# Kernel optimization log

Hardware: AMD Instinct MI355X
Metric: run time of the kernel (lower is better)

The kernel has to match this reference:

```python
import jax, jax.numpy as jnp
import numpy as np

N_NODES = 50000
N_EDGES = 600000
N_REL = 8
D_IN = 128
D_OUT = 128


def setup_inputs() -> dict:
    key = jax.random.key(0)
    ks = jax.random.split(key, 12)
    s = 1.0 / np.sqrt(D_IN)
    s2 = 1.0 / np.sqrt(2 * D_IN)
    return {
        "x": jax.random.normal(ks[0], (N_NODES, D_IN), jnp.float32),
        "src": jax.random.randint(ks[1], (N_EDGES,), 0, N_NODES, jnp.int32),
        "dst": jax.random.randint(ks[2], (N_EDGES,), 0, N_NODES, jnp.int32),
        "etype": jax.random.randint(ks[3], (N_EDGES,), 0, N_REL, jnp.int32),
        "Wrel": jax.random.normal(ks[4], (N_REL, D_IN, D_OUT), jnp.float32) * s,
        "Wloop": jax.random.normal(ks[5], (D_IN, D_OUT), jnp.float32) * s,
        "brel": jax.random.normal(ks[6], (D_OUT,), jnp.float32) * s,
        "W1": jax.random.normal(ks[7], (2 * D_IN, 2 * D_IN), jnp.float32) * s2,
        "b1": jax.random.normal(ks[8], (2 * D_IN,), jnp.float32) * s2,
        "W2": jax.random.normal(ks[9], (2 * D_IN, D_OUT), jnp.float32) * s2,
        "b2": jax.random.normal(ks[10], (D_OUT,), jnp.float32) * s2,
    }


def rel_graph_conv(x, src, dst, etype, Wrel, Wloop, brel):
    # low_mem style: transform node features once per relation, then gather per edge.
    xW = jnp.einsum('ni,rio->rno', x, Wrel)          # [R, N, D_OUT]
    msg = xW[etype, src]                              # [E, D_OUT] gather by (rel, src)
    agg = jax.ops.segment_sum(msg, dst, num_segments=N_NODES)  # scatter-add to dst
    return agg + x @ Wloop + brel                     # self-loop + bias (DGL defaults)


def reference(x, src, dst, etype, Wrel, Wloop, brel, W1, b1, W2, b2):
    mid = rel_graph_conv(x, src, dst, etype, Wrel, Wloop, brel)
    h = jnp.concatenate([x, mid], axis=1)             # [N, 2*D_IN]
    h = jax.nn.relu(h @ W1 + b1)
    return h @ W2 + b2
```

## Files before the change

kernel.cpp:

```cpp
#include <hip/hip_runtime.h>

#define N_NODES 50000
#define N_EDGES 600000
#define N_REL 8
#define NT_PAD 50176
#define N_TILES 196

typedef __attribute__((ext_vector_type(8))) short bf16x8;
typedef __attribute__((ext_vector_type(4))) float f32x4;

__device__ __forceinline__ ushort f2b(float f) {
    union { float f; unsigned u; } v; v.f = f;
    unsigned r = v.u + 0x7FFFu + ((v.u >> 16) & 1u);
    return (ushort)(r >> 16);
}
__device__ __forceinline__ float b2f(ushort s) {
    union { unsigned u; float f; } v; v.u = ((unsigned)s) << 16;
    return v.f;
}
__device__ __forceinline__ float asf(unsigned u) {
    union { unsigned u; float f; } v; v.u = u;
    return v.f;
}


__global__ void conv_f32_bf16(const float* __restrict__ in, ushort* __restrict__ outb) {
    int i = (blockIdx.x * 256 + threadIdx.x) * 4;
    float4 f = *(const float4*)(in + i);
    ushort4 o; o.x = f2b(f.x); o.y = f2b(f.y); o.z = f2b(f.z); o.w = f2b(f.w);
    *(ushort4*)(outb + i) = o;
}

__global__ void transpose_wts3(const float* __restrict__ Wloop, const float* __restrict__ Wrel,
                               const float* __restrict__ W1, const float* __restrict__ W2,
                               ushort* __restrict__ wt) {
    int y = blockIdx.y;
    if (y == 0) {
        for (int idx = blockIdx.x * 256 + threadIdx.x; idx < 128 * 1152; idx += gridDim.x * 256) {
            int c = idx / 1152, kg = idx - c * 1152;
            float v = (kg < 1024) ? Wrel[(size_t)((kg >> 7) * 128 + (kg & 127)) * 128 + c]
                                  : Wloop[(size_t)(kg - 1024) * 128 + c];
            wt[idx] = f2b(v);
        }
    } else if (y == 1) {
        for (int idx = blockIdx.x * 256 + threadIdx.x; idx < 256 * 256; idx += gridDim.x * 256) {
            int c = idx >> 8, k = idx & 255;
            wt[147456 + idx] = f2b(W1[k * 256 + c]);
        }
    } else {
        for (int idx = blockIdx.x * 256 + threadIdx.x; idx < 128 * 256; idx += gridDim.x * 256) {
            int c = idx >> 8, k = idx & 255;
            wt[212992 + idx] = f2b(W2[k * 128 + c]);
        }
    }
}

template<int NPH, int KMODE, int AS, int CTOT, int OMODE>
__global__ __launch_bounds__(256, 4) void mfma_gemm(
        const ushort* __restrict__ A0, const ushort* __restrict__ A1,
        const ushort* __restrict__ Bt, const float* __restrict__ bias,
        void* __restrict__ outv) {
    __shared__ ushort bs[2][128 * 72];
    const int t = threadIdx.x;
    const int wave = t >> 6, lane = t & 63;
    const int lr = lane & 15, lg = lane >> 4;
    const int wr = (wave >> 1) * 32, wc = (wave & 1) * 64;
    const int row0 = blockIdx.x * 64;
    const int KTOT = NPH * 64;
    const ushort* Btb = Bt + (size_t)blockIdx.y * 128 * KTOT;
    const int sgk = (t & 7) * 8;
    const int sc0 = t >> 3;

#define STAGE_LOAD(p)                                                              \
    _Pragma("unroll")                                                              \
    for (int it = 0; it < 4; ++it)                                                 \
        sreg[it] = *(const bf16x8*)(Btb + (size_t)(sc0 + it * 32) * KTOT +         \
                                    (p) * 64 + sgk);

#define STAGE_WRITE(b)                                                             \
    _Pragma("unroll")                                                              \
    for (int it = 0; it < 4; ++it)                                                 \
        *(bf16x8*)(&bs[b][(sc0 + it * 32) * 72 + sgk]) = sreg[it];

#define LOAD_AF(p, dstf)                                                           \
    {                                                                              \
        const ushort* Ap; int as_;                                                 \
        if (KMODE == 0) {                                                          \
            if ((p) < 16) { Ap = A0 + (p) * 64;        as_ = 1024; }               \
            else          { Ap = A1 + ((p) - 16) * 64; as_ = 128;  }               \
        } else { Ap = A0 + (p) * 64; as_ = AS; }                                   \
        _Pragma("unroll")                                                          \
        for (int rt = 0; rt < 2; ++rt) {                                           \
            int ar = row0 + wr + rt * 16 + lr;                                     \
            if (ar >= N_NODES) ar = 0;                                             \
            _Pragma("unroll")                                                      \
            for (int kc = 0; kc < 2; ++kc)                                         \
                dstf[rt][kc] = *(const bf16x8*)(Ap + (size_t)ar * as_ + kc * 32 + lg * 8); \
        }                                                                          \
    }

    f32x4 acc[2][4];
#pragma unroll
    for (int rt = 0; rt < 2; ++rt)
#pragma unroll
        for (int nt = 0; nt < 4; ++nt) acc[rt][nt] = (f32x4){0.f, 0.f, 0.f, 0.f};

    bf16x8 af[2][2], afn[2][2], sreg[4];

    STAGE_LOAD(0);
    LOAD_AF(0, af);
    STAGE_WRITE(0);
    __syncthreads();

#pragma unroll
    for (int p = 0; p < NPH; ++p) {
        if (p + 1 < NPH) {
            STAGE_LOAD(p + 1);
            LOAD_AF(p + 1, afn);
        }
        const ushort* bcur = bs[p & 1];
#pragma unroll
        for (int kc = 0; kc < 2; ++kc) {
            bf16x8 bf[4];
#pragma unroll
            for (int nt = 0; nt < 4; ++nt)
                bf[nt] = *(const bf16x8*)(bcur + (wc + nt * 16 + lr) * 72 + kc * 32 + lg * 8);
#pragma unroll
            for (int rt = 0; rt < 2; ++rt)
#pragma unroll
                for (int nt = 0; nt < 4; ++nt)
                    acc[rt][nt] = __builtin_amdgcn_mfma_f32_16x16x32_bf16(af[rt][kc], bf[nt], acc[rt][nt], 0, 0, 0);
        }
        if (p + 1 < NPH) STAGE_WRITE((p + 1) & 1);
        __syncthreads();
        if (p + 1 < NPH) {
#pragma unroll
            for (int rt = 0; rt < 2; ++rt)
#pragma unroll
                for (int kc = 0; kc < 2; ++kc) af[rt][kc] = afn[rt][kc];
        }
    }

    const int colbase = blockIdx.y * 128;
#pragma unroll
    for (int rt = 0; rt < 2; ++rt) {
#pragma unroll
        for (int nt = 0; nt < 4; ++nt) {
            const int col = colbase + wc + nt * 16 + lr;
            const float bv = bias[col];
#pragma unroll
            for (int j = 0; j < 4; ++j) {
                const int r = row0 + wr + rt * 16 + lg * 4 + j;
                if (r >= N_NODES) continue;
                float vv = acc[rt][nt][j] + bv;
                if (OMODE == 0) {
                    ((float*)outv)[(size_t)r * CTOT + col] = vv;
                } else {
                    ((ushort*)outv)[(size_t)r * 128 + col] = f2b(vv);
                }
            }
        }
    }
#undef STAGE_LOAD
#undef STAGE_WRITE
#undef LOAD_AF
}

__global__ __launch_bounds__(256, 2) void mlp_fused(
        const ushort* __restrict__ xbf, const ushort* __restrict__ midbf,
        const ushort* __restrict__ w1t, const ushort* __restrict__ w2t,
        const float* __restrict__ b1, const float* __restrict__ b2,
        float* __restrict__ out) {
    __shared__ ushort ldsA[256 * 72];
    __shared__ ushort ldsB[256 * 72];
    const int t = threadIdx.x;
    const int wave = t >> 6, lane = t & 63;
    const int lr = lane & 15, lg = lane >> 4;
    const int row0 = blockIdx.x * 64;
    const int sgk = (t & 7) * 8;
    const int sc0 = t >> 3;

    {
        const int wr = (wave >> 1) * 32, wc = (wave & 1) * 128;
        f32x4 acc[2][8];
#pragma unroll
        for (int rt = 0; rt < 2; ++rt)
#pragma unroll
            for (int nt = 0; nt < 8; ++nt) acc[rt][nt] = (f32x4){0.f, 0.f, 0.f, 0.f};
        bf16x8 af[2][2], afn[2][2], sreg[8];

#define S1_LOAD(p)                                                                 \
    _Pragma("unroll")                                                              \
    for (int it = 0; it < 8; ++it)                                                 \
        sreg[it] = *(const bf16x8*)(w1t + (size_t)(sc0 + it * 32) * 256 + (p) * 64 + sgk);

#define S1_WRITE(bptr)                                                             \
    _Pragma("unroll")                                                              \
    for (int it = 0; it < 8; ++it)                                                 \
        *(bf16x8*)((bptr) + (sc0 + it * 32) * 72 + sgk) = sreg[it];

#define S1_AF(p, dstf)                                                             \
    {                                                                              \
        const ushort* Ap = ((p) < 2) ? (xbf + (p) * 64) : (midbf + ((p) - 2) * 64);\
        _Pragma("unroll")                                                          \
        for (int rt = 0; rt < 2; ++rt) {                                           \
            int ar = row0 + wr + rt * 16 + lr;                                     \
            if (ar >= N_NODES) ar = 0;                                             \
            _Pragma("unroll")                                                      \
            for (int kc = 0; kc < 2; ++kc)                                         \
                dstf[rt][kc] = *(const bf16x8*)(Ap + (size_t)ar * 128 + kc * 32 + lg * 8); \
        }                                                                          \
    }

        S1_LOAD(0); S1_AF(0, af); S1_WRITE(ldsA);
        __syncthreads();
#pragma unroll
        for (int p = 0; p < 4; ++p) {
            if (p < 3) { S1_LOAD(p + 1); S1_AF(p + 1, afn); }
            const ushort* bc = (p & 1) ? ldsB : ldsA;
#pragma unroll
            for (int kc = 0; kc < 2; ++kc) {
                bf16x8 bf[8];
#pragma unroll
                for (int nt = 0; nt < 8; ++nt)
                    bf[nt] = *(const bf16x8*)(bc + (wc + nt * 16 + lr) * 72 + kc * 32 + lg * 8);
#pragma unroll
                for (int rt = 0; rt < 2; ++rt)
#pragma unroll
                    for (int nt = 0; nt < 8; ++nt)
                        acc[rt][nt] = __builtin_amdgcn_mfma_f32_16x16x32_bf16(af[rt][kc], bf[nt], acc[rt][nt], 0, 0, 0);
            }
            if (p < 3) { S1_WRITE(((p + 1) & 1) ? ldsB : ldsA); }
            __syncthreads();
            if (p < 3) {
#pragma unroll
                for (int rt = 0; rt < 2; ++rt)
#pragma unroll
                    for (int kc = 0; kc < 2; ++kc) af[rt][kc] = afn[rt][kc];
            }
        }
#pragma unroll
        for (int rt = 0; rt < 2; ++rt)
#pragma unroll
            for (int nt = 0; nt < 8; ++nt) {
                const int col = wc + nt * 16 + lr;
                const float bv = b1[col];
#pragma unroll
                for (int j = 0; j < 4; ++j) {
                    const int hr = wr + rt * 16 + lg * 4 + j;
                    ldsA[hr * 264 + col] = f2b(fmaxf(acc[rt][nt][j] + bv, 0.f));
                }
            }
#undef S1_LOAD
#undef S1_WRITE
#undef S1_AF
    }

    {
        bf16x8 sreg2[4];
#define S2_LOAD(p)                                                                 \
    _Pragma("unroll")                                                              \
    for (int it = 0; it < 4; ++it)                                                 \
        sreg2[it] = *(const bf16x8*)(w2t + (size_t)(sc0 + it * 32) * 256 + (p) * 64 + sgk);

#define S2_WRITE(half)                                                             \
    _Pragma("unroll")                                                              \
    for (int it = 0; it < 4; ++it)                                                 \
        *(bf16x8*)(ldsB + (half) * (128 * 72) + (sc0 + it * 32) * 72 + sgk) = sreg2[it];

        S2_LOAD(0); S2_WRITE(0);
        __syncthreads();

        const int wr = (wave >> 1) * 32, wc = (wave & 1) * 64;
        f32x4 acc[2][4];
#pragma unroll
        for (int rt = 0; rt < 2; ++rt)
#pragma unroll
            for (int nt = 0; nt < 4; ++nt) acc[rt][nt] = (f32x4){0.f, 0.f, 0.f, 0.f};
        bf16x8 af[2][2];

#pragma unroll
        for (int p = 0; p < 4; ++p) {
            if (p < 3) S2_LOAD(p + 1);
#pragma unroll
            for (int rt = 0; rt < 2; ++rt) {
                const int ar = wr + rt * 16 + lr;
#pragma unroll
                for (int kc = 0; kc < 2; ++kc)
                    af[rt][kc] = *(const bf16x8*)(ldsA + ar * 264 + p * 64 + kc * 32 + lg * 8);
            }
            const ushort* bc = ldsB + (p & 1) * (128 * 72);
#pragma unroll
            for (int kc = 0; kc < 2; ++kc) {
                bf16x8 bf[4];
#pragma unroll
                for (int nt = 0; nt < 4; ++nt)
                    bf[nt] = *(const bf16x8*)(bc + (wc + nt * 16 + lr) * 72 + kc * 32 + lg * 8);
#pragma unroll
                for (int rt = 0; rt < 2; ++rt)
#pragma unroll
                    for (int nt = 0; nt < 4; ++nt)
                        acc[rt][nt] = __builtin_amdgcn_mfma_f32_16x16x32_bf16(af[rt][kc], bf[nt], acc[rt][nt], 0, 0, 0);
            }
            if (p < 3) S2_WRITE((p + 1) & 1);
            __syncthreads();
        }
#pragma unroll
        for (int rt = 0; rt < 2; ++rt)
#pragma unroll
            for (int nt = 0; nt < 4; ++nt) {
                const int col = wc + nt * 16 + lr;
                const float bv = b2[col];
#pragma unroll
                for (int j = 0; j < 4; ++j) {
                    const int r = row0 + wr + rt * 16 + lg * 4 + j;
                    if (r < N_NODES)
                        out[(size_t)r * 128 + col] = acc[rt][nt][j] + bv;
                }
            }
#undef S2_LOAD
#undef S2_WRITE
    }
}


__global__ void zero_cnt(int* __restrict__ cnt) {
    int i = blockIdx.x * 256 + threadIdx.x;
    if (i < NT_PAD) cnt[i] = 0;
}

__global__ void hist_dst(const int* __restrict__ dst, int* __restrict__ cnt) {
    int e = blockIdx.x * 256 + threadIdx.x;
    if (e < N_EDGES) atomicAdd(&cnt[dst[e]], 1);
}

__global__ void scan_tiles(const int* __restrict__ cnt, int* __restrict__ tincl, int* __restrict__ bsum) {
    __shared__ int s[256];
    int i = blockIdx.x * 256 + threadIdx.x;
    int v = cnt[i];
    s[threadIdx.x] = v;
    __syncthreads();
    for (int off = 1; off < 256; off <<= 1) {
        int add = (threadIdx.x >= off) ? s[threadIdx.x - off] : 0;
        __syncthreads();
        s[threadIdx.x] += add;
        __syncthreads();
    }
    tincl[i] = s[threadIdx.x];
    if (threadIdx.x == 255) bsum[blockIdx.x] = s[255];
}

__global__ void scan_bsum(const int* __restrict__ bsum, int* __restrict__ bex) {
    __shared__ int s[256];
    int v = (threadIdx.x < N_TILES) ? bsum[threadIdx.x] : 0;
    s[threadIdx.x] = v;
    __syncthreads();
    for (int off = 1; off < 256; off <<= 1) {
        int add = (threadIdx.x >= off) ? s[threadIdx.x - off] : 0;
        __syncthreads();
        s[threadIdx.x] += add;
        __syncthreads();
    }
    if (threadIdx.x < N_TILES) bex[threadIdx.x] = s[threadIdx.x] - v;
}

__global__ void finalize_base(const int* __restrict__ cnt, const int* __restrict__ tincl,
                              const int* __restrict__ bex, int* __restrict__ base,
                              int* __restrict__ cursor) {
    int i = blockIdx.x * 256 + threadIdx.x;
    int b = tincl[i] - cnt[i] + bex[blockIdx.x];
    base[i] = b; cursor[i] = b;
}

__global__ void scatter_ids(const int* __restrict__ src, const int* __restrict__ dst,
                            const int* __restrict__ et, int* __restrict__ cursor,
                            unsigned* __restrict__ sorted) {
    int e = blockIdx.x * 256 + threadIdx.x;
    if (e >= N_EDGES) return;
    int pos = atomicAdd(&cursor[dst[e]], 1);
    sorted[pos] = ((unsigned)src[e] << 3) | (unsigned)et[e];
}


#define ACC_ADD(sd, v)                                                       \
    {                                                                        \
        float lo = asf((v) << 16);                                           \
        float hi = asf((v) & 0xffff0000u);                                   \
        switch ((sd) & 7u) {                                                 \
            case 0: a0[0] += lo; a1[0] += hi; asm volatile(""); break;       \
            case 1: a0[1] += lo; a1[1] += hi; asm volatile(""); break;       \
            case 2: a0[2] += lo; a1[2] += hi; asm volatile(""); break;       \
            case 3: a0[3] += lo; a1[3] += hi; asm volatile(""); break;       \
            case 4: a0[4] += lo; a1[4] += hi; asm volatile(""); break;       \
            case 5: a0[5] += lo; a1[5] += hi; asm volatile(""); break;       \
            case 6: a0[6] += lo; a1[6] += hi; asm volatile(""); break;       \
            default: a0[7] += lo; a1[7] += hi; asm volatile(""); break;      \
        }                                                                    \
    }

__global__ __launch_bounds__(256) void gather_agg(
        const unsigned* __restrict__ sorted, const int* __restrict__ base,
        const int* __restrict__ cnt, const ushort* __restrict__ xbf,
        ushort* __restrict__ agg) {
    const int w = threadIdx.x >> 6, lane = threadIdx.x & 63;
    const int n = blockIdx.x * 4 + w;
    const int b = base[n], c = cnt[n];
    const int loff = lane * 2;

    float a0[8], a1[8];
#pragma unroll
    for (int r = 0; r < 8; ++r) { a0[r] = 0.f; a1[r] = 0.f; }

    const unsigned* sp = sorted + b;
    int i = 0;
    for (; i + 4 <= c; i += 4) {
        unsigned s0 = __builtin_amdgcn_readfirstlane(sp[i]);
        unsigned s1 = __builtin_amdgcn_readfirstlane(sp[i + 1]);
        unsigned s2 = __builtin_amdgcn_readfirstlane(sp[i + 2]);
        unsigned s3 = __builtin_amdgcn_readfirstlane(sp[i + 3]);
        unsigned v0 = *(const unsigned*)(xbf + ((size_t)(s0 >> 3) << 7) + loff);
        unsigned v1 = *(const unsigned*)(xbf + ((size_t)(s1 >> 3) << 7) + loff);
        unsigned v2 = *(const unsigned*)(xbf + ((size_t)(s2 >> 3) << 7) + loff);
        unsigned v3 = *(const unsigned*)(xbf + ((size_t)(s3 >> 3) << 7) + loff);
        ACC_ADD(s0, v0); ACC_ADD(s1, v1); ACC_ADD(s2, v2); ACC_ADD(s3, v3);
    }
    for (; i < c; ++i) {
        unsigned sd = __builtin_amdgcn_readfirstlane(sp[i]);
        unsigned v = *(const unsigned*)(xbf + ((size_t)(sd >> 3) << 7) + loff);
        ACC_ADD(sd, v);
    }
#pragma unroll
    for (int r = 0; r < 8; ++r) {
        unsigned pk = (unsigned)f2b(a0[r]) | ((unsigned)f2b(a1[r]) << 16);
        *(unsigned*)(agg + (size_t)n * 1024 + r * 128 + loff) = pk;
    }
}
#undef ACC_ADD


extern "C" void kernel_launch(void* const* d_in, const int* in_sizes, int n_in,
                              void* d_out, int out_size, void* d_ws, size_t ws_size,
                              hipStream_t stream) {
    const float* x     = (const float*)d_in[0];
    const int*   src   = (const int*)  d_in[1];
    const int*   dst   = (const int*)  d_in[2];
    const int*   etype = (const int*)  d_in[3];
    const float* Wrel  = (const float*)d_in[4];
    const float* Wloop = (const float*)d_in[5];
    const float* brel  = (const float*)d_in[6];
    const float* W1    = (const float*)d_in[7];
    const float* b1    = (const float*)d_in[8];
    const float* W2    = (const float*)d_in[9];
    const float* b2    = (const float*)d_in[10];
    float* out = (float*)d_out;

    char* ws = (char*)d_ws;
    ushort* agg   = (ushort*)ws;
    ushort* wt    = (ushort*)(ws + 102400000);
    char* meta    = ws + 102891520;
    int* cnt      = (int*)(meta);
    int* base     = (int*)(meta + 200704);
    int* cursor   = (int*)(meta + 401408);
    int* tincl    = (int*)(meta + 602112);
    int* bsum     = (int*)(meta + 802816);
    int* bex      = (int*)(meta + 803840);
    unsigned* sorted = (unsigned*)(meta + 804864);
    ushort* xbf   = (ushort*)(ws + 106096384);
    ushort* midbf = (ushort*)(ws + 118896384);

    const ushort* wst = wt;
    const ushort* w1t = wt + 147456;
    const ushort* w2t = wt + 212992;

    conv_f32_bf16<<<6250, 256, 0, stream>>>(x, xbf);
    transpose_wts3<<<dim3(64, 3), 256, 0, stream>>>(Wloop, Wrel, W1, W2, wt);

    zero_cnt<<<N_TILES, 256, 0, stream>>>(cnt);
    hist_dst<<<(N_EDGES + 255) / 256, 256, 0, stream>>>(dst, cnt);
    scan_tiles<<<N_TILES, 256, 0, stream>>>(cnt, tincl, bsum);
    scan_bsum<<<1, 256, 0, stream>>>(bsum, bex);
    finalize_base<<<N_TILES, 256, 0, stream>>>(cnt, tincl, bex, base, cursor);
    scatter_ids<<<(N_EDGES + 255) / 256, 256, 0, stream>>>(src, dst, etype, cursor, sorted);

    gather_agg<<<N_NODES / 4, 256, 0, stream>>>(sorted, base, cnt, xbf, agg);

    mfma_gemm<18, 0, 0, 128, 4><<<dim3(782, 1), 256, 0, stream>>>(agg, xbf, wst, brel, (void*)midbf);

    mlp_fused<<<782, 256, 0, stream>>>(xbf, midbf, w1t, w2t, b1, b2, out);
}
```

Before: 207.4 us.

## Store aggregated features in MFMA fragment order for coalesced GEMM A loads

gather_agg now writes its bf16 per-relation aggregates into a pre-swizzled layout that matches the MFMA A-fragment order the GEMM expects. The first 16 K-phases of mfma_gemm then read each fragment as a contiguous 16-byte-per-lane load indexed by block, phase, wave half, row tile and k-chunk. This replaces strided row reads with a 2048-byte row stride. The cost is scattered 4-byte writes in gather_agg and a slightly larger workspace that pads rows to a multiple of 64. The workspace offsets are shifted to fit.

```diff
diff --git a/kernel.cpp b/kernel.cpp
--- a/kernel.cpp
+++ b/kernel.cpp
@@ -5,6 +5,7 @@
 #define N_REL 8
 #define NT_PAD 50176
 #define N_TILES 196
+#define NBLK 782
 
 typedef __attribute__((ext_vector_type(8))) short bf16x8;
 typedef __attribute__((ext_vector_type(4))) float f32x4;
@@ -84,18 +85,26 @@
 
 #define LOAD_AF(p, dstf)                                                           \
     {                                                                              \
-        const ushort* Ap; int as_;                                                 \
-        if (KMODE == 0) {                                                          \
-            if ((p) < 16) { Ap = A0 + (p) * 64;        as_ = 1024; }               \
-            else          { Ap = A1 + ((p) - 16) * 64; as_ = 128;  }               \
-        } else { Ap = A0 + (p) * 64; as_ = AS; }                                   \
-        _Pragma("unroll")                                                          \
-        for (int rt = 0; rt < 2; ++rt) {                                           \
-            int ar = row0 + wr + rt * 16 + lr;                                     \
-            if (ar >= N_NODES) ar = 0;                                             \
+        if (KMODE == 0 && (p) < 16) {                                              \
             _Pragma("unroll")                                                      \
-            for (int kc = 0; kc < 2; ++kc)                                         \
-                dstf[rt][kc] = *(const bf16x8*)(Ap + (size_t)ar * as_ + kc * 32 + lg * 8); \
+            for (int rt = 0; rt < 2; ++rt)                                         \
+                _Pragma("unroll")                                                  \
+                for (int kc = 0; kc < 2; ++kc)                                     \
+                    dstf[rt][kc] = *(const bf16x8*)(A0 +                           \
+                        ((((((size_t)blockIdx.x * 16 + (p)) * 2 + (wave >> 1))     \
+                           * 2 + rt) * 2 + kc) * 64 + lane) * 8);                  \
+        } else {                                                                   \
+            const ushort* Ap; int as_;                                             \
+            if (KMODE == 0) { Ap = A1 + ((p) - 16) * 64; as_ = 128; }              \
+            else            { Ap = A0 + (p) * 64;        as_ = AS;  }              \
+            _Pragma("unroll")                                                      \
+            for (int rt = 0; rt < 2; ++rt) {                                       \
+                int ar = row0 + wr + rt * 16 + lr;                                 \
+                if (ar >= N_NODES) ar = 0;                                         \
+                _Pragma("unroll")                                                  \
+                for (int kc = 0; kc < 2; ++kc)                                     \
+                    dstf[rt][kc] = *(const bf16x8*)(Ap + (size_t)ar * as_ + kc * 32 + lg * 8); \
+            }                                                                      \
         }                                                                          \
     }
 
@@ -401,7 +410,7 @@
 __global__ __launch_bounds__(256) void gather_agg(
         const unsigned* __restrict__ sorted, const int* __restrict__ base,
         const int* __restrict__ cnt, const ushort* __restrict__ xbf,
-        ushort* __restrict__ agg) {
+        ushort* __restrict__ aggF) {
     const int w = threadIdx.x >> 6, lane = threadIdx.x & 63;
     const int n = blockIdx.x * 4 + w;
     const int b = base[n], c = cnt[n];
@@ -429,10 +438,18 @@
         unsigned v = *(const unsigned*)(xbf + ((size_t)(sd >> 3) << 7) + loff);
         ACC_ADD(sd, v);
     }
+
+    const int bq = n >> 6, q = n & 63;
+    const int half = q >> 5, rt = (q >> 4) & 1, lrw = q & 15;
+    const int kcw = (lane >> 4) & 1, lgw = (lane >> 2) & 3, ew = (lane & 3) * 2;
+    const int flane = lgw * 16 + lrw;
+    const int phi = lane >> 5;
 #pragma unroll
     for (int r = 0; r < 8; ++r) {
+        const int p = r * 2 + phi;
+        size_t idx = ((((((size_t)bq * 16 + p) * 2 + half) * 2 + rt) * 2 + kcw) * 64 + flane) * 8 + ew;
         unsigned pk = (unsigned)f2b(a0[r]) | ((unsigned)f2b(a1[r]) << 16);
-        *(unsigned*)(agg + (size_t)n * 1024 + r * 128 + loff) = pk;
+        *(unsigned*)(aggF + idx) = pk;
     }
 }
 #undef ACC_ADD
@@ -455,9 +472,9 @@
     float* out = (float*)d_out;
 
     char* ws = (char*)d_ws;
-    ushort* agg   = (ushort*)ws;
-    ushort* wt    = (ushort*)(ws + 102400000);
-    char* meta    = ws + 102891520;
+    ushort* aggF  = (ushort*)ws;
+    ushort* wt    = (ushort*)(ws + 102498304);
+    char* meta    = ws + 102989824;
     int* cnt      = (int*)(meta);
     int* base     = (int*)(meta + 200704);
     int* cursor   = (int*)(meta + 401408);
@@ -465,8 +482,8 @@
     int* bsum     = (int*)(meta + 802816);
     int* bex      = (int*)(meta + 803840);
     unsigned* sorted = (unsigned*)(meta + 804864);
-    ushort* xbf   = (ushort*)(ws + 106096384);
-    ushort* midbf = (ushort*)(ws + 118896384);
+    ushort* xbf   = (ushort*)(ws + 106194688);
+    ushort* midbf = (ushort*)(ws + 118994688);
 
     const ushort* wst = wt;
     const ushort* w1t = wt + 147456;
@@ -482,9 +499,9 @@
     finalize_base<<<N_TILES, 256, 0, stream>>>(cnt, tincl, bex, base, cursor);
     scatter_ids<<<(N_EDGES + 255) / 256, 256, 0, stream>>>(src, dst, etype, cursor, sorted);
 
-    gather_agg<<<N_NODES / 4, 256, 0, stream>>>(sorted, base, cnt, xbf, agg);
-
-    mfma_gemm<18, 0, 0, 128, 4><<<dim3(782, 1), 256, 0, stream>>>(agg, xbf, wst, brel, (void*)midbf);
-
-    mlp_fused<<<782, 256, 0, stream>>>(xbf, midbf, w1t, w2t, b1, b2, out);
-}
+    gather_agg<<<N_NODES / 4, 256, 0, stream>>>(sorted, base, cnt, xbf, aggF);
+
+    mfma_gemm<18, 0, 0, 128, 4><<<dim3(NBLK, 1), 256, 0, stream>>>(aggF, xbf, wst, brel, (void*)midbf);
+
+    mlp_fused<<<NBLK, 256, 0, stream>>>(xbf, midbf, w1t, w2t, b1, b2, out);
+}
```

Result: slower. 223.6 us (+7.8%).
